# Optimization experiments

Measured on AMD Instinct MI355X. Metric: run time of the kernel, lower is better.

## Reference

```python
import jax, jax.numpy as jnp
import numpy as np

D_MODEL = 1024
NUM_HEAD = 16
D_HEAD = 64
EPS = 1e-06


def setup_inputs() -> dict:
    key = jax.random.key(0)
    ks = jax.random.split(key, 16)
    d, h = D_MODEL, 4 * D_MODEL
    s = 1.0 / np.sqrt(d)
    inp = {
        "x": jax.random.normal(ks[0], (8, 1024, d), dtype=jnp.float32),
        # LayerNorm params
        "alpha1": jnp.ones((d,), jnp.float32),
        "beta1": jnp.zeros((d,), jnp.float32),
        "alpha2": jnp.ones((d,), jnp.float32),
        "beta2": jnp.zeros((d,), jnp.float32),
        # attention projections (weights stored as [in, out])
        "w_q": jax.random.normal(ks[1], (d, d), jnp.float32) * s,
        "b_q": jnp.zeros((d,), jnp.float32),
        "w_k": jax.random.normal(ks[2], (d, d), jnp.float32) * s,
        "b_k": jnp.zeros((d,), jnp.float32),
        "w_v": jax.random.normal(ks[3], (d, d), jnp.float32) * s,
        "b_v": jnp.zeros((d,), jnp.float32),
        "w_o": jax.random.normal(ks[4], (d, d), jnp.float32) * s,
        "b_o": jnp.zeros((d,), jnp.float32),
        # MLP
        "w1": jax.random.normal(ks[5], (d, h), jnp.float32) * s,
        "b1": jnp.zeros((h,), jnp.float32),
        "w2": jax.random.normal(ks[6], (h, d), jnp.float32) * (1.0 / np.sqrt(h)),
        "b2": jnp.zeros((d,), jnp.float32),
    }
    return inp


def _layer_norm(x, alpha, beta):
    mu = jnp.mean(x, axis=-1, keepdims=True)
    # torch .var() defaults to unbiased (ddof=1) — replicate exactly
    var = jnp.var(x, axis=-1, keepdims=True, ddof=1)
    return (x - mu) / jnp.sqrt(var + EPS) * alpha + beta


def _mha(x, w_q, b_q, w_k, b_k, w_v, b_v, w_o, b_o):
    b, p, _ = x.shape
    q = (x @ w_q + b_q).reshape(b, p, NUM_HEAD, D_HEAD).transpose(0, 2, 1, 3)
    k = (x @ w_k + b_k).reshape(b, p, NUM_HEAD, D_HEAD).transpose(0, 2, 1, 3)
    v = (x @ w_v + b_v).reshape(b, p, NUM_HEAD, D_HEAD).transpose(0, 2, 1, 3)
    scores = jnp.einsum("bhqd,bhkd->bhqk", q, k) / np.sqrt(D_HEAD).astype(np.float32)
    attn = jax.nn.softmax(scores, axis=-1)
    out = jnp.einsum("bhqk,bhkd->bhqd", attn, v)
    out = out.transpose(0, 2, 1, 3).reshape(b, p, NUM_HEAD * D_HEAD)
    return out @ w_o + b_o


def reference(x, alpha1, beta1, alpha2, beta2,
              w_q, b_q, w_k, b_k, w_v, b_v, w_o, b_o,
              w1, b1, w2, b2):
    # eval mode: Dropout is identity
    x = x + _mha(_layer_norm(x, alpha1, beta1), w_q, b_q, w_k, b_k, w_v, b_v, w_o, b_o)
    h = _layer_norm(x, alpha2, beta2)
    h = jax.nn.gelu(h @ w1 + b1, approximate=False)  # nn.GELU default: exact erf
    h = h @ w2 + b2
    return x + h
```

## Files before the change

kernel.cpp:

```cpp
#include <hip/hip_runtime.h>
#include <stdint.h>

typedef float f32x4 __attribute__((ext_vector_type(4)));
typedef short s16x8 __attribute__((ext_vector_type(8)));
typedef short s16x4 __attribute__((ext_vector_type(4)));
typedef unsigned int u32x4 __attribute__((ext_vector_type(4)));

#define M_TOTAL 8192
#define DM 1024
#define HID 4096
#define SEQ 1024
#define NH 16
#define DH 64

#define BAR() __builtin_amdgcn_s_barrier()
#define VMCNT8() do { asm volatile("s_waitcnt vmcnt(8)" ::: "memory"); __builtin_amdgcn_sched_barrier(0); } while (0)
#define VMCNT0() do { asm volatile("s_waitcnt vmcnt(0)" ::: "memory"); __builtin_amdgcn_sched_barrier(0); } while (0)
#define MFMA16 __builtin_amdgcn_mfma_f32_16x16x32_bf16

__device__ __forceinline__ unsigned short f2bf(float f) {
  unsigned int u = __float_as_uint(f);
  u = (u + 0x7fffu + ((u >> 16) & 1u)) >> 16;
  return (unsigned short)u;
}

__device__ __forceinline__ void gload16(const void* g, void* l) {
  __builtin_amdgcn_global_load_lds((__attribute__((address_space(1))) void*)g,
                                   (__attribute__((address_space(3))) void*)l,
                                   16, 0, 0);
}

__device__ __forceinline__ float erf_fast(float z) {
  const float az = fabsf(z);
  const float tt = 1.0f / fmaf(0.3275911f, az, 1.0f);
  float poly = fmaf(1.061405429f, tt, -1.453152027f);
  poly = fmaf(poly, tt, 1.421413741f);
  poly = fmaf(poly, tt, -0.284496736f);
  poly = fmaf(poly, tt, 0.254829592f);
  poly *= tt;
  const float e = __expf(-az * az);
  const float r = 1.0f - poly * e;
  return (z < 0.f) ? -r : r;
}

__global__ void tcast_all(const float* __restrict__ wq, const float* __restrict__ wk,
                          const float* __restrict__ wv, const float* __restrict__ wo,
                          const float* __restrict__ w1, const float* __restrict__ w2,
                          unsigned short* __restrict__ WTqkv, unsigned short* __restrict__ WTo,
                          unsigned short* __restrict__ WT1, unsigned short* __restrict__ WT2) {
  __shared__ float tile[32][33];
  const int b = blockIdx.x;
  const float* W;
  unsigned short* WT;
  int K, N, bn, bk;
  if (b < 4096) {
    const int j = b >> 10, t2 = b & 1023;
    K = 1024; N = 1024;
    bn = t2 & 31; bk = t2 >> 5;
    W = (j == 0) ? wq : (j == 1) ? wk : (j == 2) ? wv : wo;
    WT = (j < 3) ? (WTqkv + (size_t)j * 1024 * 1024) : WTo;
  } else if (b < 8192) {
    const int t2 = b - 4096;
    K = 1024; N = 4096;
    bn = t2 & 127; bk = t2 >> 7;
    W = w1; WT = WT1;
  } else {
    const int t2 = b - 8192;
    K = 4096; N = 1024;
    bn = t2 & 31; bk = t2 >> 5;
    W = w2; WT = WT2;
  }
  const int tx = threadIdx.x, ty = threadIdx.y;
#pragma unroll
  for (int i = 0; i < 32; i += 8)
    tile[ty + i][tx] = W[(size_t)(bk * 32 + ty + i) * N + bn * 32 + tx];
  __syncthreads();
#pragma unroll
  for (int i = 0; i < 32; i += 8)
    WT[(size_t)(bn * 32 + ty + i) * K + bk * 32 + tx] = f2bf(tile[tx][ty + i]);
}

__global__ __launch_bounds__(256)
void ln_kernel(const float* __restrict__ x, const float* __restrict__ alpha,
               const float* __restrict__ beta, unsigned short* __restrict__ out) {
  const int row = blockIdx.x;
  const int t = threadIdx.x;
  const int w = t >> 6, lane = t & 63;
  const float4 v = ((const float4*)(x + (size_t)row * DM))[t];

  float s = v.x + v.y + v.z + v.w;
#pragma unroll
  for (int off = 32; off; off >>= 1) s += __shfl_xor(s, off, 64);
  __shared__ float red1[4];
  __shared__ float red2[4];
  if (lane == 0) red1[w] = s;
  __syncthreads();
  const float mu = (red1[0] + red1[1] + red1[2] + red1[3]) * (1.f / 1024.f);

  const float dx = v.x - mu, dy = v.y - mu, dz = v.z - mu, dw = v.w - mu;
  float sq = dx * dx + dy * dy + dz * dz + dw * dw;
#pragma unroll
  for (int off = 32; off; off >>= 1) sq += __shfl_xor(sq, off, 64);
  if (lane == 0) red2[w] = sq;
  __syncthreads();
  const float var = (red2[0] + red2[1] + red2[2] + red2[3]) * (1.f / 1023.f);
  const float rstd = rsqrtf(var + 1e-6f);

  const float4 a = ((const float4*)alpha)[t];
  const float4 b = ((const float4*)beta)[t];
  s16x4 o;
  o[0] = (short)f2bf(dx * rstd * a.x + b.x);
  o[1] = (short)f2bf(dy * rstd * a.y + b.y);
  o[2] = (short)f2bf(dz * rstd * a.z + b.z);
  o[3] = (short)f2bf(dw * rstd * a.w + b.w);
  *(s16x4*)(out + (size_t)row * DM + 4 * t) = o;
}

template <int MODE>
__device__ __forceinline__ void epi_store(int m, int n, float v, int Nout,
                                          unsigned short* __restrict__ obf, float* of,
                                          const float* res,
                                          const float* __restrict__ bias0) {
  if (MODE == 1) {
    v += bias0[n] + res[(size_t)m * Nout + n];
    of[(size_t)m * Nout + n] = v;
  } else {
    v += bias0[n];
    const float gv = 0.5f * v * (1.0f + erf_fast(v * 0.70710678118654752f));
    obf[(size_t)m * Nout + n] = f2bf(gv);
  }
}

template <int MODE>
__global__ __launch_bounds__(256, 2)
void gemmk(const unsigned short* __restrict__ A, const unsigned short* __restrict__ B,
           int K, int Nout,
           unsigned short* __restrict__ obf, float* of, const float* res,
           const float* __restrict__ bias0, const float* __restrict__ bias1,
           const float* __restrict__ bias2) {
  __shared__ __attribute__((aligned(16))) unsigned short sA[2][128 * 64];
  __shared__ __attribute__((aligned(16))) unsigned short sB[2][128 * 64];
  const int t = threadIdx.x;
  const int lane = t & 63, wid = t >> 6;
  const int g = lane >> 4, r = lane & 15;
  const int wm = wid >> 1, wn = wid & 1;

  const int L = blockIdx.y * gridDim.x + blockIdx.x;
  const int nwg = gridDim.x * gridDim.y;
  const int chunk = nwg >> 3;
  const int ncols = chunk >> 6;
  const int denom = ncols << 3;
  const int xcd = L & 7, li = L >> 3;
  const int sst = li / denom, wst = li % denom;
  const int by = sst * 8 + (wst & 7);
  const int bx = xcd * ncols + (wst >> 3);
  const int m0 = by * 128, n0 = bx * 128;

  const unsigned short* Ab = A + (size_t)m0 * K;
  const unsigned short* Bb = B + (size_t)n0 * K;

  const int rb = r & 7;
  const int slot0 = (g ^ rb) * 16;
  const int slot1 = ((4 + g) ^ rb) * 16;

  f32x4 acc[4][4];
#pragma unroll
  for (int i2 = 0; i2 < 4; ++i2)
#pragma unroll
    for (int j = 0; j < 4; ++j) acc[i2][j] = (f32x4){0.f, 0.f, 0.f, 0.f};

  auto stage = [&](int buf, int kt) {
#pragma unroll
    for (int s2 = 0; s2 < 4; ++s2) {
      const int f = s2 * 256 + t;
      const int row = f >> 3, c = f & 7;
      const int u = c ^ (row & 7);
      gload16(Ab + (size_t)row * K + kt * 64 + u * 8, &sA[buf][(size_t)row * 64 + c * 8]);
      gload16(Bb + (size_t)row * K + kt * 64 + u * 8, &sB[buf][(size_t)row * 64 + c * 8]);
    }
  };

  const int NT = K >> 6;
  stage(0, 0);
  stage(1, (NT > 1) ? 1 : 0);
  VMCNT8();
  BAR();

  for (int tt = 0; tt < NT; ++tt) {
    const int cur = tt & 1;
    const char* sAc = (const char*)&sA[cur][0];
    const char* sBc = (const char*)&sB[cur][0];

    s16x8 av[4][2], bv[4][2];
#pragma unroll
    for (int i2 = 0; i2 < 4; ++i2) {
      const int rbyte = (wm * 64 + i2 * 16 + r) * 128;
      av[i2][0] = *(const s16x8*)(sAc + rbyte + slot0);
      av[i2][1] = *(const s16x8*)(sAc + rbyte + slot1);
    }
#pragma unroll
    for (int n = 0; n < 4; ++n) {
      const int rbyte = (wn * 64 + n * 16 + r) * 128;
      bv[n][0] = *(const s16x8*)(sBc + rbyte + slot0);
      bv[n][1] = *(const s16x8*)(sBc + rbyte + slot1);
    }
#pragma unroll
    for (int i2 = 0; i2 < 4; ++i2)
#pragma unroll
      for (int n = 0; n < 4; ++n) {
        acc[i2][n] = MFMA16(av[i2][0], bv[n][0], acc[i2][n], 0, 0, 0);
        acc[i2][n] = MFMA16(av[i2][1], bv[n][1], acc[i2][n], 0, 0, 0);
      }

    BAR();
    const int tp2 = (tt + 2 < NT) ? tt + 2 : NT - 1;
    stage(cur, tp2);
    VMCNT8();
    BAR();
  }

  VMCNT0();

  if (MODE == 0) {
    const int which = n0 >> 10;
    const int hn = ((n0 & 1023) + wn * 64) >> 6;
    const int mwave = m0 + wm * 64;
    const int b = mwave >> 10, s_wb = mwave & 1023;
    if (which == 2) {
      BAR();
      unsigned short* tl = (unsigned short*)&sA[0][0] + (size_t)wid * (64 * 64);
#pragma unroll
      for (int i2 = 0; i2 < 4; ++i2)
#pragma unroll
        for (int nf = 0; nf < 4; ++nf) {
          const int d = nf * 16 + r;
          const float bias = bias2[hn * 64 + d];
          s16x4 o;
#pragma unroll
          for (int j = 0; j < 4; ++j) o[j] = (short)f2bf(acc[i2][nf][j] + bias);
          *(s16x4*)&tl[d * 64 + i2 * 16 + 4 * g] = o;
        }
      unsigned short* vout = obf + (size_t)2 * (M_TOTAL * DM) +
                             ((size_t)(b * NH + hn) * DH) * SEQ + s_wb;
#pragma unroll
      for (int p2 = 0; p2 < 16; ++p2) {
        const int d = p2 * 4 + g;
        const s16x4 v = *(const s16x4*)&tl[d * 64 + 4 * r];
        *(s16x4*)(vout + (size_t)d * SEQ + 4 * r) = v;
      }
    } else {
#pragma unroll
      for (int i2 = 0; i2 < 4; ++i2)
#pragma unroll
        for (int nf = 0; nf < 4; ++nf) {
          const int d = nf * 16 + r;
          const float bias = (which == 0) ? bias0[hn * 64 + d] : bias1[hn * 64 + d];
          const int s_base = s_wb + i2 * 16 + 4 * g;
#pragma unroll
          for (int j = 0; j < 4; ++j) {
            float v = acc[i2][nf][j] + bias;
            if (which == 0) v *= 0.125f;
            obf[(size_t)which * (M_TOTAL * DM) +
                (((size_t)(b * NH + hn) * SEQ + (s_base + j)) * DH + d)] = f2bf(v);
          }
        }
    }
  } else {
#pragma unroll
    for (int i2 = 0; i2 < 4; ++i2)
#pragma unroll
      for (int j = 0; j < 4; ++j) {
        const int m = m0 + wm * 64 + i2 * 16 + 4 * g + j;
#pragma unroll
        for (int nf = 0; nf < 4; ++nf) {
          const int n = n0 + wn * 64 + nf * 16 + r;
          epi_store<MODE>(m, n, acc[i2][nf][j], Nout, obf, of, res, bias0);
        }
      }
  }
}

__global__ __launch_bounds__(256)
void attn_kernel(const unsigned short* __restrict__ QKV,
                 unsigned short* __restrict__ O) {
  const unsigned short* Qg = QKV;
  const unsigned short* Kg = QKV + (size_t)M_TOTAL * DM;
  const unsigned short* VTg = QKV + 2 * (size_t)M_TOTAL * DM;
  const int bh = blockIdx.y;
  const int q0 = blockIdx.x * 64;
  const int t = threadIdx.x, w = t >> 6, lane = t & 63;
  const int g = lane >> 4, r = lane & 15;
  const unsigned short* Qb = Qg + (size_t)bh * SEQ * DH;
  const unsigned short* Kb = Kg + (size_t)bh * SEQ * DH;
  const unsigned short* VTb = VTg + (size_t)bh * DH * SEQ;

  __shared__ __attribute__((aligned(16))) unsigned short sK[2][64 * 64];
  __shared__ __attribute__((aligned(16))) unsigned short sV[2][64 * 64];

  s16x8 qf[2];
  {
    const unsigned short* qrow = Qb + (size_t)(q0 + w * 16 + r) * DH;
    qf[0] = *(const s16x8*)(qrow + g * 8);
    qf[1] = *(const s16x8*)(qrow + 32 + g * 8);
  }

  f32x4 oacc[4];
#pragma unroll
  for (int i = 0; i < 4; ++i) oacc[i] = (f32x4){0.f, 0.f, 0.f, 0.f};
  float mrun = -1e30f, lrun = 0.f;

  auto stage = [&](int buf, int kt) {
#pragma unroll
    for (int s2 = 0; s2 < 2; ++s2) {
      const int f = s2 * 256 + t;
      const int row = f >> 3, u = (f & 7) ^ (row & 7);
      gload16(Kb + (size_t)(kt * 64 + row) * DH + u * 8, &sK[buf][f * 8]);
      gload16(VTb + (size_t)row * SEQ + kt * 64 + u * 8, &sV[buf][f * 8]);
    }
  };

  stage(0, 0);
  __syncthreads();

  for (int kt = 0; kt < SEQ / 64; ++kt) {
    const int cur = kt & 1;
    if (kt < SEQ / 64 - 1) stage(cur ^ 1, kt + 1);

    f32x4 sc[4];
#pragma unroll
    for (int nf = 0; nf < 4; ++nf) {
      sc[nf] = (f32x4){0.f, 0.f, 0.f, 0.f};
      const int rowk = nf * 16 + r;
#pragma unroll
      for (int ks = 0; ks < 2; ++ks) {
        const int u = (4 * ks + g) ^ (rowk & 7);
        const s16x8 kf = *(const s16x8*)&sK[cur][rowk * 64 + u * 8];
        sc[nf] = __builtin_amdgcn_mfma_f32_16x16x32_bf16(kf, qf[ks], sc[nf], 0, 0, 0);
      }
    }

    float pm = -1e30f;
#pragma unroll
    for (int nf = 0; nf < 4; ++nf)
#pragma unroll
      for (int j = 0; j < 4; ++j) pm = fmaxf(pm, sc[nf][j]);
    pm = fmaxf(pm, __shfl_xor(pm, 16, 64));
    pm = fmaxf(pm, __shfl_xor(pm, 32, 64));

    if (!__all(pm - mrun <= 8.0f)) {
      const float mnew = fmaxf(mrun, pm);
      const float alpha = __expf(mrun - mnew);
      mrun = mnew;
      lrun *= alpha;
      float ao[4];
#pragma unroll
      for (int j = 0; j < 4; ++j) ao[j] = __shfl(alpha, 4 * g + j, 64);
#pragma unroll
      for (int nf2 = 0; nf2 < 4; ++nf2)
#pragma unroll
        for (int j = 0; j < 4; ++j) oacc[nf2][j] *= ao[j];
    }

    float p[4][4];
    float ps = 0.f;
#pragma unroll
    for (int nf = 0; nf < 4; ++nf)
#pragma unroll
      for (int j = 0; j < 4; ++j) {
        p[nf][j] = __expf(sc[nf][j] - mrun);
        ps += p[nf][j];
      }
    ps += __shfl_xor(ps, 16, 64);
    ps += __shfl_xor(ps, 32, 64);
    lrun += ps;

    unsigned int pk[4][2];
#pragma unroll
    for (int nf = 0; nf < 4; ++nf)
#pragma unroll
      for (int jp = 0; jp < 2; ++jp)
        pk[nf][jp] = (unsigned int)f2bf(p[nf][2 * jp]) |
                     ((unsigned int)f2bf(p[nf][2 * jp + 1]) << 16);

    unsigned int pa32[2][4];
#pragma unroll
    for (int ks = 0; ks < 2; ++ks)
#pragma unroll
      for (int q2 = 0; q2 < 4; ++q2) {
        const int src = r + 32 * (g & 1) + 16 * (q2 >> 1);
        const unsigned int a = (unsigned int)__shfl((int)pk[2 * ks][q2 & 1], src, 64);
        const unsigned int b = (unsigned int)__shfl((int)pk[2 * ks + 1][q2 & 1], src, 64);
        pa32[ks][q2] = (g >> 1) ? b : a;
      }
    s16x8 pa[2];
#pragma unroll
    for (int ks = 0; ks < 2; ++ks) {
      u32x4 pw;
      pw[0] = pa32[ks][0]; pw[1] = pa32[ks][1];
      pw[2] = pa32[ks][2]; pw[3] = pa32[ks][3];
      pa[ks] = __builtin_bit_cast(s16x8, pw);
    }

#pragma unroll
    for (int nf2 = 0; nf2 < 4; ++nf2) {
      const int rowd = nf2 * 16 + r;
#pragma unroll
      for (int ks = 0; ks < 2; ++ks) {
        const int u = (4 * ks + g) ^ (rowd & 7);
        const s16x8 vb = *(const s16x8*)&sV[cur][rowd * 64 + u * 8];
        oacc[nf2] = __builtin_amdgcn_mfma_f32_16x16x32_bf16(pa[ks], vb, oacc[nf2], 0, 0, 0);
      }
    }
    __syncthreads();
  }

  const int b = bh >> 4, h = bh & 15;
  const float linv = 1.f / lrun;
#pragma unroll
  for (int j = 0; j < 4; ++j) {
    const float lo = __shfl(linv, 4 * g + j, 64);
    const int q = q0 + w * 16 + 4 * g + j;
    const size_t orow = ((size_t)(b * SEQ + q)) * DM + h * DH;
#pragma unroll
    for (int nf2 = 0; nf2 < 4; ++nf2)
      O[orow + nf2 * 16 + r] = f2bf(oacc[nf2][j] * lo);
  }
}

extern "C" void kernel_launch(void* const* d_in, const int* in_sizes, int n_in,
                              void* d_out, int out_size, void* d_ws, size_t ws_size,
                              hipStream_t stream) {
  const float* x   = (const float*)d_in[0];
  const float* al1 = (const float*)d_in[1];
  const float* be1 = (const float*)d_in[2];
  const float* al2 = (const float*)d_in[3];
  const float* be2 = (const float*)d_in[4];
  const float* wq  = (const float*)d_in[5];
  const float* bq  = (const float*)d_in[6];
  const float* wk  = (const float*)d_in[7];
  const float* bk  = (const float*)d_in[8];
  const float* wv  = (const float*)d_in[9];
  const float* bv  = (const float*)d_in[10];
  const float* wo  = (const float*)d_in[11];
  const float* bo  = (const float*)d_in[12];
  const float* w1  = (const float*)d_in[13];
  const float* b1  = (const float*)d_in[14];
  const float* w2  = (const float*)d_in[15];
  const float* b2  = (const float*)d_in[16];
  float* dout = (float*)d_out;

  unsigned short* ws = (unsigned short*)d_ws;
  size_t off = 0;
  auto alloc = [&](size_t n) { unsigned short* p = ws + off; off += n; return p; };
  unsigned short* WTqkv = alloc((size_t)3072 * 1024);
  unsigned short* WTo   = alloc((size_t)1024 * 1024);
  unsigned short* WT1   = alloc((size_t)4096 * 1024);
  unsigned short* WT2   = alloc((size_t)1024 * 4096);
  unsigned short* xn    = alloc((size_t)M_TOTAL * DM);
  unsigned short* QKVb  = alloc((size_t)3 * M_TOTAL * DM);
  unsigned short* attn  = alloc((size_t)M_TOTAL * DM);
  unsigned short* h1    = alloc((size_t)M_TOTAL * HID);
  (void)ws_size; (void)in_sizes; (void)n_in; (void)out_size;

  tcast_all<<<12288, dim3(32, 8), 0, stream>>>(wq, wk, wv, wo, w1, w2,
                                               WTqkv, WTo, WT1, WT2);

  ln_kernel<<<M_TOTAL, 256, 0, stream>>>(x, al1, be1, xn);
  gemmk<0><<<dim3(24, 64), 256, 0, stream>>>(xn, WTqkv, 1024, 3072,
                                             QKVb, nullptr, nullptr, bq, bk, bv);
  attn_kernel<<<dim3(16, 128), 256, 0, stream>>>(QKVb, attn);
  gemmk<1><<<dim3(8, 64), 256, 0, stream>>>(attn, WTo, 1024, 1024,
                                            nullptr, dout, x, bo, nullptr, nullptr);
  ln_kernel<<<M_TOTAL, 256, 0, stream>>>(dout, al2, be2, xn);
  gemmk<2><<<dim3(32, 64), 256, 0, stream>>>(xn, WT1, 1024, 4096,
                                             h1, nullptr, nullptr, b1, nullptr, nullptr);
  gemmk<1><<<dim3(8, 64), 256, 0, stream>>>(h1, WT2, 4096, 1024,
                                            nullptr, dout, dout, b2, nullptr, nullptr);
}
```

Before: 408.2 us.

## Add single-buffered GEMM variant with higher occupancy for QKV and FC1

```diff
diff --git a/kernel.cpp b/kernel.cpp
--- a/kernel.cpp
+++ b/kernel.cpp
@@ -131,6 +131,19 @@
   }
 }
 
+__device__ __forceinline__ void supertile_map(int& m0, int& n0) {
+  const int L = blockIdx.y * gridDim.x + blockIdx.x;
+  const int nwg = gridDim.x * gridDim.y;
+  const int chunk = nwg >> 3;
+  const int ncols = chunk >> 6;
+  const int denom = ncols << 3;
+  const int xcd = L & 7, li = L >> 3;
+  const int sst = li / denom, wst = li % denom;
+  const int by = sst * 8 + (wst & 7);
+  const int bx = xcd * ncols + (wst >> 3);
+  m0 = by * 128; n0 = bx * 128;
+}
+
 template <int MODE>
 __global__ __launch_bounds__(256, 2)
 void gemmk(const unsigned short* __restrict__ A, const unsigned short* __restrict__ B,
@@ -145,16 +158,8 @@
   const int g = lane >> 4, r = lane & 15;
   const int wm = wid >> 1, wn = wid & 1;
 
-  const int L = blockIdx.y * gridDim.x + blockIdx.x;
-  const int nwg = gridDim.x * gridDim.y;
-  const int chunk = nwg >> 3;
-  const int ncols = chunk >> 6;
-  const int denom = ncols << 3;
-  const int xcd = L & 7, li = L >> 3;
-  const int sst = li / denom, wst = li % denom;
-  const int by = sst * 8 + (wst & 7);
-  const int bx = xcd * ncols + (wst >> 3);
-  const int m0 = by * 128, n0 = bx * 128;
+  int m0, n0;
+  supertile_map(m0, n0);
 
   const unsigned short* Ab = A + (size_t)m0 * K;
   const unsigned short* Bb = B + (size_t)n0 * K;
@@ -221,14 +226,102 @@
 
   VMCNT0();
 
+#pragma unroll
+  for (int i2 = 0; i2 < 4; ++i2)
+#pragma unroll
+    for (int j = 0; j < 4; ++j) {
+      const int m = m0 + wm * 64 + i2 * 16 + 4 * g + j;
+#pragma unroll
+      for (int nf = 0; nf < 4; ++nf) {
+        const int n = n0 + wn * 64 + nf * 16 + r;
+        epi_store<MODE>(m, n, acc[i2][nf][j], Nout, obf, of, res, bias0);
+      }
+    }
+}
+
+template <int MODE>
+__global__ __launch_bounds__(256, 4)
+void gemms(const unsigned short* __restrict__ A, const unsigned short* __restrict__ B,
+           int K, int Nout,
+           unsigned short* __restrict__ obf, float* of, const float* res,
+           const float* __restrict__ bias0, const float* __restrict__ bias1,
+           const float* __restrict__ bias2) {
+  __shared__ __attribute__((aligned(16))) unsigned short sM[2][128 * 64];
+  const int t = threadIdx.x;
+  const int lane = t & 63, wid = t >> 6;
+  const int g = lane >> 4, r = lane & 15;
+  const int wm = wid >> 1, wn = wid & 1;
+
+  int m0, n0;
+  supertile_map(m0, n0);
+
+  const unsigned short* Ab = A + (size_t)m0 * K;
+  const unsigned short* Bb = B + (size_t)n0 * K;
+
+  const int rb = r & 7;
+  const int slot0 = (g ^ rb) * 16;
+  const int slot1 = ((4 + g) ^ rb) * 16;
+
+  f32x4 acc[4][4];
+#pragma unroll
+  for (int i2 = 0; i2 < 4; ++i2)
+#pragma unroll
+    for (int j = 0; j < 4; ++j) acc[i2][j] = (f32x4){0.f, 0.f, 0.f, 0.f};
+
+  auto stage = [&](int kt) {
+#pragma unroll
+    for (int s2 = 0; s2 < 4; ++s2) {
+      const int f = s2 * 256 + t;
+      const int row = f >> 3, c = f & 7;
+      const int u = c ^ (row & 7);
+      gload16(Ab + (size_t)row * K + kt * 64 + u * 8, &sM[0][(size_t)row * 64 + c * 8]);
+      gload16(Bb + (size_t)row * K + kt * 64 + u * 8, &sM[1][(size_t)row * 64 + c * 8]);
+    }
+  };
+
+  const int NT = K >> 6;
+  stage(0);
+  VMCNT0();
+  BAR();
+
+  for (int tt = 0; tt < NT; ++tt) {
+    const char* sAc = (const char*)&sM[0][0];
+    const char* sBc = (const char*)&sM[1][0];
+
+    s16x8 av[4][2], bv[4][2];
+#pragma unroll
+    for (int i2 = 0; i2 < 4; ++i2) {
+      const int rbyte = (wm * 64 + i2 * 16 + r) * 128;
+      av[i2][0] = *(const s16x8*)(sAc + rbyte + slot0);
+      av[i2][1] = *(const s16x8*)(sAc + rbyte + slot1);
+    }
+#pragma unroll
+    for (int n = 0; n < 4; ++n) {
+      const int rbyte = (wn * 64 + n * 16 + r) * 128;
+      bv[n][0] = *(const s16x8*)(sBc + rbyte + slot0);
+      bv[n][1] = *(const s16x8*)(sBc + rbyte + slot1);
+    }
+#pragma unroll
+    for (int i2 = 0; i2 < 4; ++i2)
+#pragma unroll
+      for (int n = 0; n < 4; ++n) {
+        acc[i2][n] = MFMA16(av[i2][0], bv[n][0], acc[i2][n], 0, 0, 0);
+        acc[i2][n] = MFMA16(av[i2][1], bv[n][1], acc[i2][n], 0, 0, 0);
+      }
+
+    BAR();
+    stage((tt + 1 < NT) ? tt + 1 : tt);
+    VMCNT0();
+    BAR();
+  }
+
   if (MODE == 0) {
     const int which = n0 >> 10;
     const int hn = ((n0 & 1023) + wn * 64) >> 6;
     const int mwave = m0 + wm * 64;
     const int b = mwave >> 10, s_wb = mwave & 1023;
     if (which == 2) {
-      BAR();
-      unsigned short* tl = (unsigned short*)&sA[0][0] + (size_t)wid * (64 * 64);
+      unsigned short* tl = (unsigned short*)&sM[0][0] + (size_t)wid * (64 * 64);
 #pragma unroll
       for (int i2 = 0; i2 < 4; ++i2)
 #pragma unroll
@@ -466,13 +559,13 @@
                                                WTqkv, WTo, WT1, WT2);
 
   ln_kernel<<<M_TOTAL, 256, 0, stream>>>(x, al1, be1, xn);
-  gemmk<0><<<dim3(24, 64), 256, 0, stream>>>(xn, WTqkv, 1024, 3072,
+  gemms<0><<<dim3(24, 64), 256, 0, stream>>>(xn, WTqkv, 1024, 3072,
                                              QKVb, nullptr, nullptr, bq, bk, bv);
   attn_kernel<<<dim3(16, 128), 256, 0, stream>>>(QKVb, attn);
   gemmk<1><<<dim3(8, 64), 256, 0, stream>>>(attn, WTo, 1024, 1024,
                                             nullptr, dout, x, bo, nullptr, nullptr);
   ln_kernel<<<M_TOTAL, 256, 0, stream>>>(dout, al2, be2, xn);
-  gemmk<2><<<dim3(32, 64), 256, 0, stream>>>(xn, WT1, 1024, 4096,
+  gemms<2><<<dim3(32, 64), 256, 0, stream>>>(xn, WT1, 1024, 4096,
                                              h1, nullptr, nullptr, b1, nullptr, nullptr);
   gemmk<1><<<dim3(8, 64), 256, 0, stream>>>(h1, WT2, 4096, 1024,
                                             nullptr, dout, dout, b2, nullptr, nullptr);
```

Result: no change. 401.2 us (-1.7%).
